# Optimization experiments

Hardware: AMD Instinct MI355X
Metric: run time of the kernel (lower is better)

## Reference

```python
import jax, jax.numpy as jnp
import numpy as np

B, S, D, H = 4, 2048, 1024, 16
DH = D // H  # 64


def setup_inputs() -> dict:
    key = jax.random.key(0)
    ks = jax.random.split(key, 8)
    sc = 1.0 / np.sqrt(D)
    return {
        "hidden_states": jax.random.normal(ks[0], (B, S, D), jnp.float32),
        "attention_mask": jnp.zeros((B, 1, 1, S), jnp.float32),
        "Wq": jax.random.normal(ks[1], (D, D), jnp.float32) * sc,
        "bq": jnp.zeros((D,), jnp.float32),
        "Wk": jax.random.normal(ks[2], (D, D), jnp.float32) * sc,
        "bk": jnp.zeros((D,), jnp.float32),
        "Wv": jax.random.normal(ks[3], (D, D), jnp.float32) * sc,
        "bv": jnp.zeros((D,), jnp.float32),
    }


def _heads(x):
    # [B,S,D] -> [B,H,S,DH]
    b, s, _ = x.shape
    return x.reshape(b, s, H, DH).transpose(0, 2, 1, 3)


def reference(hidden_states, attention_mask, Wq, bq, Wk, bk, Wv, bv):
    q = _heads(hidden_states @ Wq + bq)
    k = _heads(hidden_states @ Wk + bk)
    v = _heads(hidden_states @ Wv + bv)
    scores = jnp.einsum('bhqd,bhkd->bhqk', q, k) / jnp.sqrt(jnp.float32(DH))
    scores = scores + attention_mask  # additive mask, broadcast
    probs = jax.nn.softmax(scores, axis=-1)  # dropout is identity in eval
    out = jnp.einsum('bhqk,bhkd->bhqd', probs, v)
    b, h, s, dh = out.shape
    return out.transpose(0, 2, 1, 3).reshape(b, s, h * dh)
```

## Files before the change

kernel.cpp:

```cpp
#include <hip/hip_runtime.h>
#include <hip/hip_bf16.h>
#include <cstdint>

typedef _Float16 f16;
typedef f16 f16x8 __attribute__((ext_vector_type(8)));
typedef f16 f16x4 __attribute__((ext_vector_type(4)));
typedef float f32x4 __attribute__((ext_vector_type(4)));

#define MFMA16(a, b, c) __builtin_amdgcn_mfma_f32_16x16x32_f16((a), (b), (c), 0, 0, 0)
#define MFMA16K16(a, b, c) __builtin_amdgcn_mfma_f32_16x16x16f16((a), (b), (c), 0, 0, 0)

constexpr int Bc = 4, Sc = 2048, Dc = 1024, Hc = 16, DHc = 64;

typedef __attribute__((address_space(1))) const uint32_t gbl_u32;
typedef __attribute__((address_space(3))) uint32_t lds_u32;
__device__ __forceinline__ void gld_lds16(const void* g, void* l) {
  __builtin_amdgcn_global_load_lds((gbl_u32*)g, (lds_u32*)l, 16, 0, 0);
}

__global__ __launch_bounds__(256) void cast_w_kernel(
    const float* __restrict__ Wq, const float* __restrict__ Wk,
    const float* __restrict__ Wv, f16* __restrict__ Wt) {
  __shared__ __align__(16) f16 T[64][66];
  const int z = blockIdx.z;
  const float* W = (z == 0) ? Wq : (z == 1) ? Wk : Wv;
  const int n0 = blockIdx.x * 64, k0 = blockIdx.y * 64;
  const int t = threadIdx.x;
#pragma unroll
  for (int p = 0; p < 4; p++) {
    int idx = t + p * 256;
    int r = idx >> 4, c = idx & 15;
    float4 v = *(const float4*)(W + (size_t)(k0 + r) * Dc + n0 + c * 4);
    T[r][c * 4 + 0] = (f16)v.x;
    T[r][c * 4 + 1] = (f16)v.y;
    T[r][c * 4 + 2] = (f16)v.z;
    T[r][c * 4 + 3] = (f16)v.w;
  }
  __syncthreads();
#pragma unroll
  for (int p = 0; p < 2; p++) {
    int idx = t + p * 256;
    int n = idx >> 3, c = idx & 7;
    f16x8 tmp;
#pragma unroll
    for (int j = 0; j < 8; j++) tmp[j] = T[c * 8 + j][n];
    *(f16x8*)(Wt + ((size_t)z * Dc + n0 + n) * Dc + k0 + c * 8) = tmp;
  }
}

__global__ __launch_bounds__(256) void cast_x_kernel(const float* __restrict__ X,
                                                     f16* __restrict__ X16) {
  size_t i = ((size_t)blockIdx.x * 256 + threadIdx.x) * 8;
  float4 a = *(const float4*)(X + i);
  float4 b = *(const float4*)(X + i + 4);
  f16x8 h;
  h[0] = (f16)a.x; h[1] = (f16)a.y; h[2] = (f16)a.z; h[3] = (f16)a.w;
  h[4] = (f16)b.x; h[5] = (f16)b.y; h[6] = (f16)b.z; h[7] = (f16)b.w;
  *(f16x8*)(X16 + i) = h;
}

__global__ __launch_bounds__(256) void qkv_gemm_kernel(
    const f16* __restrict__ X16, const f16* __restrict__ Wt,
    const float* __restrict__ bq, const float* __restrict__ bk,
    const float* __restrict__ bv, f16* __restrict__ Qo, f16* __restrict__ Ko,
    f16* __restrict__ Vo) {
  const int z = blockIdx.z;
  const f16* W = Wt + (size_t)z * Dc * Dc;
  const float* bias = (z == 0) ? bq : (z == 1) ? bk : bv;

  const int n0 = blockIdx.x * 128, m0 = blockIdx.y * 128;
  __shared__ __align__(16) f16 Xs[128 * 32];
  __shared__ __align__(16) f16 Ws[128 * 32];

  const int t = threadIdx.x;
  const int wave = t >> 6, lane = t & 63;
  const int l16 = lane & 15, quad = lane >> 4;
  const int wm = (wave >> 1) * 64, wn = (wave & 1) * 64;

  f32x4 acc[4][4];
#pragma unroll
  for (int i = 0; i < 4; i++)
#pragma unroll
    for (int j = 0; j < 4; j++) acc[i][j] = (f32x4){0.f, 0.f, 0.f, 0.f};

  for (int k0 = 0; k0 < Dc; k0 += 32) {
#pragma unroll
    for (int p = 0; p < 2; p++) {
      int cb = p * 256 + wave * 64;
      int chunk = cb + lane;
      int row = chunk >> 2, c8 = (chunk & 3) * 8;
      gld_lds16(X16 + (size_t)(m0 + row) * Dc + k0 + c8, (f16*)Xs + (size_t)cb * 8);
      gld_lds16(W + (size_t)(n0 + row) * Dc + k0 + c8, (f16*)Ws + (size_t)cb * 8);
    }
    __syncthreads();

    f16x8 aF[4], bF[4];
#pragma unroll
    for (int mt = 0; mt < 4; mt++)
      aF[mt] = *(const f16x8*)(&Xs[(wm + mt * 16 + l16) * 32 + quad * 8]);
#pragma unroll
    for (int nt = 0; nt < 4; nt++)
      bF[nt] = *(const f16x8*)(&Ws[(wn + nt * 16 + l16) * 32 + quad * 8]);
#pragma unroll
    for (int mt = 0; mt < 4; mt++)
#pragma unroll
      for (int nt = 0; nt < 4; nt++)
        acc[mt][nt] = MFMA16(aF[mt], bF[nt], acc[mt][nt]);
    __syncthreads();
  }

#pragma unroll
  for (int nt = 0; nt < 4; nt++) {
    int col = n0 + wn + nt * 16 + l16;
    float bval = bias[col];
    int h = col >> 6, d = col & 63;
    if (z == 2) {
#pragma unroll
      for (int mt = 0; mt < 4; mt++) {
        int m = m0 + wm + mt * 16 + quad * 4;
        int b = m >> 11, sbase = m & 2047;
        f16x4 pk;
#pragma unroll
        for (int r = 0; r < 4; r++) pk[r] = (f16)(acc[mt][nt][r] + bval);
        *(f16x4*)(Vo + (((size_t)(b * Hc + h)) * DHc + d) * Sc + sbase) = pk;
      }
    } else {
      const float sc = (z == 0) ? 0.125f : 1.0f;
      f16* O = (z == 0) ? Qo : Ko;
#pragma unroll
      for (int mt = 0; mt < 4; mt++) {
#pragma unroll
        for (int r = 0; r < 4; r++) {
          int m = m0 + wm + mt * 16 + quad * 4 + r;
          int b = m >> 11, s = m & 2047;
          O[(((size_t)(b * Hc + h)) * Sc + s) * DHc + d] =
              (f16)((acc[mt][nt][r] + bval) * sc);
        }
      }
    }
  }
}

__global__ __launch_bounds__(256) void flash_kernel(
    const f16* __restrict__ Q, const f16* __restrict__ K,
    const f16* __restrict__ Vt, const float* __restrict__ mask,
    float* __restrict__ out) {
  const int bh = blockIdx.y;
  const int b = bh >> 4, h = bh & 15;
  const int t = threadIdx.x;
  const int wave = t >> 6, lane = t & 63;
  const int l16 = lane & 15, quad = lane >> 4;
  const int qbase = blockIdx.x * 128 + wave * 32;

  __shared__ __align__(16) f16 Ks[2][4096];
  __shared__ __align__(16) f16 Vs[2][4096];

  const f16* Kb = K + (size_t)bh * Sc * DHc;
  const f16* Vb = Vt + (size_t)bh * DHc * Sc;
  const float* mrow = mask + (size_t)b * Sc;

  const int qsw8 = (quad ^ ((l16 >> 1) & 3)) * 8;
  const int vsw = (l16 >> 1) & 3;

  auto stageKV = [&](int c0, int buf) {
#pragma unroll
    for (int p = 0; p < 2; p++) {
      int cb = p * 256 + wave * 64;
      int i = cb + lane;
      int half = i >> 8, row = (i >> 2) & 63, q8 = i & 3;
      int q8g = q8 ^ ((row >> 1) & 3);
      gld_lds16(Kb + (size_t)(c0 + row) * DHc + half * 32 + q8g * 8,
                &Ks[buf][cb * 8]);
      gld_lds16(Vb + (size_t)row * Sc + c0 + half * 32 + q8g * 8,
                &Vs[buf][cb * 8]);
    }
  };

  f16x8 qa[2][2];
#pragma unroll
  for (int mt = 0; mt < 2; mt++) {
    const f16* qb = Q + ((size_t)bh * Sc + qbase + mt * 16 + l16) * DHc;
    qa[mt][0] = *(const f16x8*)(qb + quad * 8);
    qa[mt][1] = *(const f16x8*)(qb + 32 + quad * 8);
  }

  stageKV(0, 0);
  __syncthreads();

  float l_acc[2] = {0.f, 0.f};
  f32x4 o[2][4];
#pragma unroll
  for (int mt = 0; mt < 2; mt++)
#pragma unroll
    for (int dt = 0; dt < 4; dt++) o[mt][dt] = (f32x4){0.f, 0.f, 0.f, 0.f};

  for (int c = 0; c < 32; c++) {
    const int buf = c & 1;
    float4 mv[4];
#pragma unroll
    for (int nt = 0; nt < 4; nt++)
      mv[nt] = *(const float4*)(mrow + c * 64 + nt * 16 + quad * 4);
    if (c < 31) stageKV((c + 1) * 64, buf ^ 1);

    f16x8 ka[4][2];
#pragma unroll
    for (int nt = 0; nt < 4; nt++) {
      int rb = (nt * 16 + l16) * 32 + qsw8;
      ka[nt][0] = *(const f16x8*)(&Ks[buf][rb]);
      ka[nt][1] = *(const f16x8*)(&Ks[buf][2048 + rb]);
    }

    f32x4 s0[4], s1[4];
#pragma unroll
    for (int nt = 0; nt < 4; nt++) {
      f32x4 a = (f32x4){mv[nt].x, mv[nt].y, mv[nt].z, mv[nt].w};
      a = MFMA16(ka[nt][0], qa[0][0], a);
      a = MFMA16(ka[nt][1], qa[0][1], a);
      s0[nt] = a;
      f32x4 a2 = (f32x4){mv[nt].x, mv[nt].y, mv[nt].z, mv[nt].w};
      a2 = MFMA16(ka[nt][0], qa[1][0], a2);
      a2 = MFMA16(ka[nt][1], qa[1][1], a2);
      s1[nt] = a2;
    }

    f16x4 pA[2][4];
#pragma unroll
    for (int nt = 0; nt < 4; nt++) {
      float ls0 = 0.f, ls1 = 0.f;
      f16x4 p0, p1;
#pragma unroll
      for (int r = 0; r < 4; r++) {
        float e0 = __expf(s0[nt][r]);
        float e1 = __expf(s1[nt][r]);
        ls0 += e0; ls1 += e1;
        p0[r] = (f16)e0; p1[r] = (f16)e1;
      }
      pA[0][nt] = p0; pA[1][nt] = p1;
      l_acc[0] += ls0; l_acc[1] += ls1;
    }

#pragma unroll
    for (int dt = 0; dt < 4; dt++) {
      int dh = dt * 16 + l16;
#pragma unroll
      for (int nt = 0; nt < 4; nt++) {
        int q8g = (((nt & 1) * 2 + (quad >> 1)) ^ vsw) * 8;
        f16x4 vB = *(const f16x4*)(
            &Vs[buf][(nt >> 1) * 2048 + dh * 32 + q8g + (quad & 1) * 4]);
        o[0][dt] = MFMA16K16(pA[0][nt], vB, o[0][dt]);
        o[1][dt] = MFMA16K16(pA[1][nt], vB, o[1][dt]);
      }
    }

    __syncthreads();
  }

#pragma unroll
  for (int mt = 0; mt < 2; mt++) {
    l_acc[mt] += __shfl_xor(l_acc[mt], 16);
    l_acc[mt] += __shfl_xor(l_acc[mt], 32);
  }
#pragma unroll
  for (int mt = 0; mt < 2; mt++) {
    float inv[4];
#pragma unroll
    for (int r = 0; r < 4; r++)
      inv[r] = 1.0f / __shfl(l_acc[mt], quad * 4 + r);
#pragma unroll
    for (int dt = 0; dt < 4; dt++) {
      int col = h * 64 + dt * 16 + l16;
#pragma unroll
      for (int r = 0; r < 4; r++) {
        int row = qbase + mt * 16 + quad * 4 + r;
        out[((size_t)b * Sc + row) * Dc + col] = o[mt][dt][r] * inv[r];
      }
    }
  }
}

extern "C" void kernel_launch(void* const* d_in, const int* in_sizes, int n_in,
                              void* d_out, int out_size, void* d_ws,
                              size_t ws_size, hipStream_t stream) {
  (void)in_sizes; (void)n_in; (void)out_size; (void)ws_size;
  const float* hidden = (const float*)d_in[0];
  const float* mask   = (const float*)d_in[1];
  const float* Wq     = (const float*)d_in[2];
  const float* bq     = (const float*)d_in[3];
  const float* Wk     = (const float*)d_in[4];
  const float* bk     = (const float*)d_in[5];
  const float* Wv     = (const float*)d_in[6];
  const float* bv     = (const float*)d_in[7];
  float* out = (float*)d_out;

  uint8_t* w = (uint8_t*)d_ws;
  f16* Wt   = (f16*)(w);
  f16* X16  = (f16*)(w + (size_t)6 * 1024 * 1024);
  f16* Q16  = (f16*)(w + (size_t)22 * 1024 * 1024);
  f16* K16  = (f16*)(w + (size_t)38 * 1024 * 1024);
  f16* Vt16 = (f16*)(w + (size_t)54 * 1024 * 1024);

  cast_w_kernel<<<dim3(16, 16, 3), 256, 0, stream>>>(Wq, Wk, Wv, Wt);
  cast_x_kernel<<<4096, 256, 0, stream>>>(hidden, X16);
  qkv_gemm_kernel<<<dim3(8, 64, 3), 256, 0, stream>>>(X16, Wt, bq, bk, bv,
                                                      Q16, K16, Vt16);
  flash_kernel<<<dim3(16, 64), 256, 0, stream>>>(Q16, K16, Vt16, mask, out);
}
```

Baseline: 286.2 us.

## Permute K rows so PV product uses 16x16x32 MFMA with f16x8 V loads

Reorders which key rows are staged into each LDS slot so that the score accumulator layout matches the K=32 operand layout of the 16x16x32 MFMA. P can then be packed into f16x8 fragments and the PV product uses half as many MFMA instructions, with wider 16-byte V reads from LDS. The mask loads are re-indexed to follow the permuted key order. Correctness depends on the permutation, mask indexing and V swizzle all staying consistent.

```diff
diff --git a/kernel.cpp b/kernel.cpp
--- a/kernel.cpp
+++ b/kernel.cpp
@@ -8,7 +8,6 @@
 typedef float f32x4 __attribute__((ext_vector_type(4)));
 
 #define MFMA16(a, b, c) __builtin_amdgcn_mfma_f32_16x16x32_f16((a), (b), (c), 0, 0, 0)
-#define MFMA16K16(a, b, c) __builtin_amdgcn_mfma_f32_16x16x16f16((a), (b), (c), 0, 0, 0)
 
 constexpr int Bc = 4, Sc = 2048, Dc = 1024, Hc = 16, DHc = 64;
 
@@ -160,7 +159,6 @@
   const float* mrow = mask + (size_t)b * Sc;
 
   const int qsw8 = (quad ^ ((l16 >> 1) & 3)) * 8;
-  const int vsw = (l16 >> 1) & 3;
 
   auto stageKV = [&](int c0, int buf) {
 #pragma unroll
@@ -169,7 +167,8 @@
       int i = cb + lane;
       int half = i >> 8, row = (i >> 2) & 63, q8 = i & 3;
       int q8g = q8 ^ ((row >> 1) & 3);
-      gld_lds16(Kb + (size_t)(c0 + row) * DHc + half * 32 + q8g * 8,
+      int g = (row & 32) | ((row & 12) << 1) | ((row & 16) >> 2) | (row & 3);
+      gld_lds16(Kb + (size_t)(c0 + g) * DHc + half * 32 + q8g * 8,
                 &Ks[buf][cb * 8]);
       gld_lds16(Vb + (size_t)row * Sc + c0 + half * 32 + q8g * 8,
                 &Vs[buf][cb * 8]);
@@ -199,7 +198,8 @@
     float4 mv[4];
 #pragma unroll
     for (int nt = 0; nt < 4; nt++)
-      mv[nt] = *(const float4*)(mrow + c * 64 + nt * 16 + quad * 4);
+      mv[nt] = *(const float4*)(mrow + c * 64 + (nt >> 1) * 32 + quad * 8 +
+                                (nt & 1) * 4);
     if (c < 31) stageKV((c + 1) * 64, buf ^ 1);
 
     f16x8 ka[4][2];
@@ -223,33 +223,36 @@
       s1[nt] = a2;
     }
 
-    f16x4 pA[2][4];
-#pragma unroll
-    for (int nt = 0; nt < 4; nt++) {
-      float ls0 = 0.f, ls1 = 0.f;
-      f16x4 p0, p1;
-#pragma unroll
-      for (int r = 0; r < 4; r++) {
-        float e0 = __expf(s0[nt][r]);
-        float e1 = __expf(s1[nt][r]);
-        ls0 += e0; ls1 += e1;
-        p0[r] = (f16)e0; p1[r] = (f16)e1;
+    f16x8 pa[2][2];
+#pragma unroll
+    for (int blk = 0; blk < 2; blk++) {
+      f16x8 p0, p1;
+#pragma unroll
+      for (int half = 0; half < 2; half++) {
+        int nt = blk * 2 + half;
+        float ls0 = 0.f, ls1 = 0.f;
+#pragma unroll
+        for (int r = 0; r < 4; r++) {
+          float e0 = __expf(s0[nt][r]);
+          float e1 = __expf(s1[nt][r]);
+          ls0 += e0; ls1 += e1;
+          p0[half * 4 + r] = (f16)e0;
+          p1[half * 4 + r] = (f16)e1;
+        }
+        l_acc[0] += ls0; l_acc[1] += ls1;
       }
-      pA[0][nt] = p0; pA[1][nt] = p1;
-      l_acc[0] += ls0; l_acc[1] += ls1;
+      pa[0][blk] = p0; pa[1][blk] = p1;
     }
 
 #pragma unroll
     for (int dt = 0; dt < 4; dt++) {
-      int dh = dt * 16 + l16;
-#pragma unroll
-      for (int nt = 0; nt < 4; nt++) {
-        int q8g = (((nt & 1) * 2 + (quad >> 1)) ^ vsw) * 8;
-        f16x4 vB = *(const f16x4*)(
-            &Vs[buf][(nt >> 1) * 2048 + dh * 32 + q8g + (quad & 1) * 4]);
-        o[0][dt] = MFMA16K16(pA[0][nt], vB, o[0][dt]);
-        o[1][dt] = MFMA16K16(pA[1][nt], vB, o[1][dt]);
-      }
+      int rb = (dt * 16 + l16) * 32 + qsw8;
+      f16x8 v0 = *(const f16x8*)(&Vs[buf][rb]);
+      f16x8 v1 = *(const f16x8*)(&Vs[buf][2048 + rb]);
+      o[0][dt] = MFMA16(pa[0][0], v0, o[0][dt]);
+      o[0][dt] = MFMA16(pa[0][1], v1, o[0][dt]);
+      o[1][dt] = MFMA16(pa[1][0], v0, o[1][dt]);
+      o[1][dt] = MFMA16(pa[1][1], v1, o[1][dt]);
     }
 
     __syncthreads();
```

After: 279.0 us. 2.5% less time.
